# Optimization experiments

Hardware: AMD Instinct MI355X
Metric: run time of the kernel (lower is better)

The kernel has to match this reference:

```python
import jax, jax.numpy as jnp
import numpy as np

BOND_D = 4    # disentangler bond dim (hard-coded 4 in torch init)
BOND_I = 16   # isometry bond dim (bond_dim kwarg)
F = 2         # feature_dim = 2*nCh, nCh=1 -> [x, 1-x] embedding
LEVELS = [128, 64, 32, 16, 8, 4]
NUM_CLASSES = 10
BATCH = 16


def setup_inputs() -> dict:
    key = jax.random.key(0)
    ks = iter(jax.random.split(key, 128))
    inp = {}
    inp["x"] = jax.random.uniform(next(ks), (BATCH, 1, 128, 128), dtype=jnp.float32)

    def mps_params(P, D, O):
        A = 0.2 * jax.random.normal(next(ks), (P, 4, F, D, D), dtype=jnp.float32)
        v = 0.2 * jax.random.normal(next(ks), (P, D), dtype=jnp.float32)
        w = 0.2 * jax.random.normal(next(ks), (P, D, O), dtype=jnp.float32)
        return A, v, w

    for l, H in enumerate(LEVELS, start=1):
        Pd = ((H - 2) // 2) ** 2   # number of disentangler patches
        Pi = (H // 2) ** 2         # number of isometry patches
        inp[f"d{l}A"], inp[f"d{l}v"], inp[f"d{l}w"] = mps_params(Pd, BOND_D, 4)
        inp[f"i{l}A"], inp[f"i{l}v"], inp[f"i{l}w"] = mps_params(Pi, BOND_I, 1)
    inp["fA"], inp["fv"], inp["fw"] = mps_params(1, BOND_I, NUM_CLASSES)
    return inp


def _patches(x):
    # x: [b, H, W] (H, W even) -> [b, (H/2)*(W/2), 4], same site order as
    # torch unfold(2,2,2).unfold(3,2,2).reshape(..., 4)
    b, H, W = x.shape
    return x.reshape(b, H // 2, 2, W // 2, 2).transpose(0, 1, 3, 2, 4).reshape(b, -1, 4)


def _unpatch(y, nh, nw):
    # y: [b, nh*nw, 4] -> [b, 2*nh, 2*nw], inverse spatial placement of 2x2 blocks
    b = y.shape[0]
    return y.reshape(b, nh, nw, 2, 2).transpose(0, 1, 3, 2, 4).reshape(b, 2 * nh, 2 * nw)


def _mps(patches, A, v, w):
    # Batched per-patch ReLU-MPS over 4 sites.
    # patches [b,P,4], A [P,4,F,D,D], v [P,D], w [P,D,O] -> [b,P,O]
    phi = jnp.stack([patches, 1.0 - patches], axis=-1)          # [b,P,4,F]
    M = jnp.einsum('bpsf,psfij->bpsij', phi, A)                 # [b,P,4,D,D]
    vec = jnp.einsum('pi,bpij->bpj', v, M[:, :, 0])             # [b,P,D]
    for s in range(1, 4):
        vec = jnp.einsum('bpi,bpij->bpj', vec, M[:, :, s])
    return jax.nn.relu(jnp.einsum('bpi,pio->bpo', vec, w))


def _level(x, dA, dv, dw, iA, iv, iw):
    # One MERA layer: disentangle shifted interior patches, write back, then
    # isometry-pool the full grid 2x2 -> 1.
    b, H, W = x.shape
    nh = (H - 2) // 2
    y = _mps(_patches(x[:, 1:-1, 1:-1]), dA, dv, dw)            # [b, nh*nh, 4]
    x = x.at[:, 1:-1, 1:-1].set(_unpatch(y, nh, nh))
    y2 = _mps(_patches(x), iA, iv, iw)                          # [b, (H/2)^2, 1]
    return y2.reshape(b, H // 2, W // 2)


def reference(x, d1A, d1v, d1w, i1A, i1v, i1w,
              d2A, d2v, d2w, i2A, i2v, i2w,
              d3A, d3v, d3w, i3A, i3v, i3w,
              d4A, d4v, d4w, i4A, i4v, i4w,
              d5A, d5v, d5w, i5A, i5v, i5w,
              d6A, d6v, d6w, i6A, i6v, i6w,
              fA, fv, fw):
    h = x[:, 0]  # nCh = 1
    levels = [(d1A, d1v, d1w, i1A, i1v, i1w), (d2A, d2v, d2w, i2A, i2v, i2w),
              (d3A, d3v, d3w, i3A, i3v, i3w), (d4A, d4v, d4w, i4A, i4v, i4w),
              (d5A, d5v, d5w, i5A, i5v, i5w), (d6A, d6v, d6w, i6A, i6v, i6w)]
    for p in levels:
        h = _level(h, *p)
    flat = h.reshape(h.shape[0], 1, 4)         # final 2x2 grid -> 4 sites
    return _mps(flat, fA, fv, fw)[:, 0]        # [b, NUM_CLASSES]
```

## Files before the change

### kernel.cpp

```cpp
#include <hip/hip_runtime.h>

#define BATCH 16

template <int CTRL>
__device__ __forceinline__ float qperm(float x) {
  int xi = __float_as_int(x);
  return __int_as_float(__builtin_amdgcn_update_dpp(xi, xi, CTRL, 0xF, 0xF, true));
}

__device__ __forceinline__ float4 f4fma(float s, float4 a, float4 c) {
  c.x = fmaf(s, a.x, c.x);
  c.y = fmaf(s, a.y, c.y);
  c.z = fmaf(s, a.z, c.z);
  c.w = fmaf(s, a.w, c.w);
  return c;
}

__device__ __forceinline__ void mps16_chain(const float* __restrict__ A,
                                            int jq, const float tt[4],
                                            float vec[4]) {
#pragma unroll
  for (int s = 0; s < 4; s++) {
    const float4* A0v = (const float4*)(A + s * 512) + jq;
    const float4* A1v = A0v + 64;
    float4 q0 = {0.f, 0.f, 0.f, 0.f}, q1 = {0.f, 0.f, 0.f, 0.f};
#define ISTEP(i)                                         \
  {                                                      \
    float sv = qperm<(((i) >> 2) * 0x55)>(vec[(i) & 3]); \
    q0 = f4fma(sv, A0v[(i) * 4], q0);                    \
    q1 = f4fma(sv, A1v[(i) * 4], q1);                    \
  }
    ISTEP(0) ISTEP(1) ISTEP(2) ISTEP(3)
    ISTEP(4) ISTEP(5) ISTEP(6) ISTEP(7)
    ISTEP(8) ISTEP(9) ISTEP(10) ISTEP(11)
    ISTEP(12) ISTEP(13) ISTEP(14) ISTEP(15)
#undef ISTEP
    float ph = tt[s], om = 1.0f - ph;
    vec[0] = ph * q0.x + om * q1.x;
    vec[1] = ph * q0.y + om * q1.y;
    vec[2] = ph * q0.z + om * q1.z;
    vec[3] = ph * q0.w + om * q1.w;
  }
}

template <int H, int XS>
__device__ __forceinline__ float fused_di_quad(
    const float* __restrict__ xb, int p, int jq,
    const float* __restrict__ dA, const float* __restrict__ dv,
    const float* __restrict__ dw,
    const float* __restrict__ iA, const float* __restrict__ iv,
    const float* __restrict__ iw) {
  constexpr int NH = (H - 2) / 2;
  constexpr int W2 = H / 2;
  int pi = p / W2, pj = p % W2;
  int r = 2 * pi + (jq >> 1), c = 2 * pj + (jq & 1);
  float tcell;
  bool border = (r == 0) | (r == H - 1) | (c == 0) | (c == H - 1);
  if (border) {
    tcell = xb[(r * H + c) * XS];
  } else {
    int dpi = (r - 1) >> 1, dpj = (c - 1) >> 1;
    int sd = ((r - 1) & 1) * 2 + ((c - 1) & 1);
    int dp = dpi * NH + dpj;
    int R0 = 1 + 2 * dpi, C0 = 1 + 2 * dpj;
    float tins[4];
    tins[0] = xb[(R0 * H + C0) * XS];
    tins[1] = xb[(R0 * H + C0 + 1) * XS];
    tins[2] = xb[((R0 + 1) * H + C0) * XS];
    tins[3] = xb[((R0 + 1) * H + C0 + 1) * XS];
    const float4* Av = (const float4*)(dA + dp * 128);
    float4 dvv = *(const float4*)(dv + dp * 4);
    float v0 = dvv.x, v1 = dvv.y, v2 = dvv.z, v3 = dvv.w;
#pragma unroll
    for (int s = 0; s < 4; s++) {
      const float4* A0 = Av + s * 8;
      float4 q0 = {0.f, 0.f, 0.f, 0.f}, q1 = {0.f, 0.f, 0.f, 0.f};
      q0 = f4fma(v0, A0[0], q0);
      q0 = f4fma(v1, A0[1], q0);
      q0 = f4fma(v2, A0[2], q0);
      q0 = f4fma(v3, A0[3], q0);
      q1 = f4fma(v0, A0[4], q1);
      q1 = f4fma(v1, A0[5], q1);
      q1 = f4fma(v2, A0[6], q1);
      q1 = f4fma(v3, A0[7], q1);
      float ph = tins[s], om = 1.0f - ph;
      v0 = ph * q0.x + om * q1.x;
      v1 = ph * q0.y + om * q1.y;
      v2 = ph * q0.z + om * q1.z;
      v3 = ph * q0.w + om * q1.w;
    }
    const float* wp = dw + dp * 16 + sd;
    float y = v0 * wp[0];
    y = fmaf(v1, wp[4], y);
    y = fmaf(v2, wp[8], y);
    y = fmaf(v3, wp[12], y);
    tcell = fmaxf(y, 0.0f);
  }
  float tt[4];
  tt[0] = qperm<0x00>(tcell);
  tt[1] = qperm<0x55>(tcell);
  tt[2] = qperm<0xAA>(tcell);
  tt[3] = qperm<0xFF>(tcell);
  float4 vv = *(const float4*)(iv + p * 16 + 4 * jq);
  float vec[4] = {vv.x, vv.y, vv.z, vv.w};
  mps16_chain(iA + (size_t)p * 2048, jq, tt, vec);
  float4 wv = *(const float4*)(iw + p * 16 + 4 * jq);
  float partial = vec[0] * wv.x;
  partial = fmaf(vec[1], wv.y, partial);
  partial = fmaf(vec[2], wv.z, partial);
  partial = fmaf(vec[3], wv.w, partial);
  partial += qperm<0xB1>(partial);
  partial += qperm<0x4E>(partial);
  return fmaxf(partial, 0.0f);
}

template <int H, int BP, int XS>
__global__ __launch_bounds__(256) void level_kernel(
    const float* __restrict__ xin, float* __restrict__ hn,
    const float* __restrict__ dA, const float* __restrict__ dv,
    const float* __restrict__ dw, const float* __restrict__ iA,
    const float* __restrict__ iv, const float* __restrict__ iw) {
  int tid = threadIdx.x;
  int jq = tid & 3;
  int b = (tid >> 2) & 15;
  int p = blockIdx.x * BP + (tid >> 6);
  const float* xb = (XS == 1) ? (xin + b * H * H) : (xin + b);
  float o = fused_di_quad<H, XS>(xb, p, jq, dA, dv, dw, iA, iv, iw);
  if (jq == 0) hn[p * 16 + b] = o;
}

struct TailArgs {
  const float* h3;
  const float* in[21];
  float* out;
};

__global__ __launch_bounds__(256) void tail_kernel(TailArgs a) {
  __shared__ float x4[256];
  __shared__ float x5[64];
  __shared__ float x6[16];
  __shared__ float h6[4];
  int b = blockIdx.x;
  int tid = threadIdx.x;
  x4[tid] = a.h3[tid * 16 + b];
  __syncthreads();
  {
    int jq = tid & 3, p = tid >> 2;
    float o = fused_di_quad<16, 1>(x4, p, jq, a.in[0], a.in[1], a.in[2],
                                   a.in[3], a.in[4], a.in[5]);
    if (jq == 0) x5[p] = o;
  }
  __syncthreads();
  if (tid < 64) {
    int jq = tid & 3, p = tid >> 2;
    float o = fused_di_quad<8, 1>(x5, p, jq, a.in[6], a.in[7], a.in[8],
                                  a.in[9], a.in[10], a.in[11]);
    if (jq == 0) x6[p] = o;
  }
  __syncthreads();
  if (tid < 16) {
    int jq = tid & 3, p = tid >> 2;
    float o = fused_di_quad<4, 1>(x6, p, jq, a.in[12], a.in[13], a.in[14],
                                  a.in[15], a.in[16], a.in[17]);
    if (jq == 0) h6[p] = o;
  }
  __syncthreads();
  if (tid < 4) {
    int jq = tid;
    const float* fA = a.in[18];
    const float* fv = a.in[19];
    const float* fw = a.in[20];
    float tt[4] = {h6[0], h6[1], h6[2], h6[3]};
    float4 vv = *(const float4*)(fv + 4 * jq);
    float vec[4] = {vv.x, vv.y, vv.z, vv.w};
    mps16_chain(fA, jq, tt, vec);
    float acc[10];
#pragma unroll
    for (int o = 0; o < 10; o++) acc[o] = 0.f;
#pragma unroll
    for (int k = 0; k < 4; k++)
#pragma unroll
      for (int o = 0; o < 10; o++)
        acc[o] = fmaf(vec[k], fw[(4 * jq + k) * 10 + o], acc[o]);
#pragma unroll
    for (int o = 0; o < 10; o++) {
      acc[o] += qperm<0xB1>(acc[o]);
      acc[o] += qperm<0x4E>(acc[o]);
    }
    if (jq == 0) {
#pragma unroll
      for (int o = 0; o < 10; o++) a.out[b * 10 + o] = fmaxf(acc[o], 0.0f);
    }
  }
}

extern "C" void kernel_launch(void* const* d_in, const int* in_sizes, int n_in,
                              void* d_out, int out_size, void* d_ws, size_t ws_size,
                              hipStream_t stream) {
  const float* x = (const float*)d_in[0];
  float* ws = (float*)d_ws;
  float* h1 = ws;
  float* h2 = h1 + 65536;
  float* h3 = h2 + 16384;

  level_kernel<128, 4, 1><<<1024, 256, 0, stream>>>(
      x, h1, (const float*)d_in[1], (const float*)d_in[2],
      (const float*)d_in[3], (const float*)d_in[4], (const float*)d_in[5],
      (const float*)d_in[6]);
  level_kernel<64, 4, 16><<<256, 256, 0, stream>>>(
      h1, h2, (const float*)d_in[7], (const float*)d_in[8],
      (const float*)d_in[9], (const float*)d_in[10], (const float*)d_in[11],
      (const float*)d_in[12]);
  level_kernel<32, 1, 16><<<256, 64, 0, stream>>>(
      h2, h3, (const float*)d_in[13], (const float*)d_in[14],
      (const float*)d_in[15], (const float*)d_in[16], (const float*)d_in[17],
      (const float*)d_in[18]);

  TailArgs ta;
  ta.h3 = h3;
  for (int i = 0; i < 21; i++) ta.in[i] = (const float*)d_in[19 + i];
  ta.out = (float*)d_out;
  tail_kernel<<<BATCH, 256, 0, stream>>>(ta);
}
```

Baseline: 222.7 us.

## Stage per-block MPS parameters in LDS, transpose input, restructure level/tail kernels

Each level block now cooperatively loads its isometry tensors and the neighbouring disentangler tensors into shared memory with coalesced float4 loads, then runs the chains out of LDS. Previously every thread read scattered global memory. A new transpose kernel puts the input in batch-innermost layout so level 1 can use the same path. Level 4 moves from the single-block-per-batch tail into the grid-wide level kernel, and the tail now handles four batches per block over levels 5-6 and the final MPS. This adds a kernel launch and LDS pressure, and duplicates disentangler loads at block halos.

```diff
diff --git a/kernel.cpp b/kernel.cpp
--- a/kernel.cpp
+++ b/kernel.cpp
@@ -16,9 +16,8 @@
   return c;
 }
 
-__device__ __forceinline__ void mps16_chain(const float* __restrict__ A,
-                                            int jq, const float tt[4],
-                                            float vec[4]) {
+__device__ __forceinline__ void mps16_chain(const float* A, int jq,
+                                            const float tt[4], float vec[4]) {
 #pragma unroll
   for (int s = 0; s < 4; s++) {
     const float4* A0v = (const float4*)(A + s * 512) + jq;
@@ -114,63 +113,212 @@
   return fmaxf(partial, 0.0f);
 }
 
-template <int H, int BP, int XS>
+#define OFF_IA 0
+#define OFF_IV 8192
+#define OFF_IW 8256
+#define OFF_DA 8320
+#define OFF_DV 9640
+#define OFF_DW 9680
+#define LDS_TOT 9840
+
+template <int H>
 __global__ __launch_bounds__(256) void level_kernel(
-    const float* __restrict__ xin, float* __restrict__ hn,
+    const float* __restrict__ xT, float* __restrict__ hn,
     const float* __restrict__ dA, const float* __restrict__ dv,
     const float* __restrict__ dw, const float* __restrict__ iA,
     const float* __restrict__ iv, const float* __restrict__ iw) {
+  constexpr int W2 = H / 2, NH = (H - 2) / 2;
+  __shared__ __align__(16) float lds[LDS_TOT];
+  float4* l4 = (float4*)lds;
+  const int tid = threadIdx.x;
+  const int p0 = blockIdx.x * 4;
+  const int pi = p0 / W2, pj0 = p0 % W2;
+  const int jq = tid & 3, b = (tid >> 2) & 15, w = tid >> 6;
+  const int pj = pj0 + w;
+  const int r = 2 * pi + (jq >> 1), c = 2 * pj + (jq & 1);
+  const bool border = (r == 0) | (r == H - 1) | (c == 0) | (c == H - 1);
+  const int dpi = (r - 1) >> 1, dpj = (c - 1) >> 1;
+
+  float xv0, xv1, xv2, xv3;
+  if (border) {
+    xv0 = xT[(r * H + c) * 16 + b];
+  } else {
+    int R0 = 1 + 2 * dpi, C0 = 1 + 2 * dpj;
+    xv0 = xT[(R0 * H + C0) * 16 + b];
+    xv1 = xT[(R0 * H + C0 + 1) * 16 + b];
+    xv2 = xT[((R0 + 1) * H + C0) * 16 + b];
+    xv3 = xT[((R0 + 1) * H + C0 + 1) * 16 + b];
+  }
+
+  {
+    const float4* iA4 = (const float4*)iA + p0 * 512;
+    float4 ra[8];
+#pragma unroll
+    for (int k = 0; k < 8; k++) ra[k] = iA4[tid + k * 256];
+
+    float4 rd0, rd1;
+    int sl0, gr0, sl1, gr1;
+    const bool md1 = tid < 64;
+    {
+      int g = tid;
+      int rs = g / 160, rem = g % 160, cs = rem / 32;
+      gr0 = rem % 32;
+      int di = min(max(pi - 1 + rs, 0), NH - 1);
+      int dj = min(max(pj0 - 1 + cs, 0), NH - 1);
+      sl0 = rs * 5 + cs;
+      rd0 = *((const float4*)dA + (di * NH + dj) * 32 + gr0);
+    }
+    if (md1) {
+      int g = tid + 256;
+      int rs = g / 160, rem = g % 160, cs = rem / 32;
+      gr1 = rem % 32;
+      int di = min(max(pi - 1 + rs, 0), NH - 1);
+      int dj = min(max(pj0 - 1 + cs, 0), NH - 1);
+      sl1 = rs * 5 + cs;
+      rd1 = *((const float4*)dA + (di * NH + dj) * 32 + gr1);
+    }
+    float4 rv;
+    const bool mv = tid < 10;
+    if (mv) {
+      int rs = tid / 5, cs = tid % 5;
+      int di = min(max(pi - 1 + rs, 0), NH - 1);
+      int dj = min(max(pj0 - 1 + cs, 0), NH - 1);
+      rv = *((const float4*)dv + (di * NH + dj));
+    }
+    float4 rw;
+    const bool mw = tid < 40;
+    if (mw) {
+      int rs = tid / 20, rem = tid % 20, cs = rem / 4, gr = rem % 4;
+      int di = min(max(pi - 1 + rs, 0), NH - 1);
+      int dj = min(max(pj0 - 1 + cs, 0), NH - 1);
+      rw = *((const float4*)dw + (di * NH + dj) * 4 + gr);
+    }
+    float4 rvv, rww;
+    const bool mi = tid < 16;
+    if (mi) {
+      rvv = *((const float4*)iv + p0 * 4 + tid);
+      rww = *((const float4*)iw + p0 * 4 + tid);
+    }
+#pragma unroll
+    for (int k = 0; k < 8; k++) l4[OFF_IA / 4 + tid + k * 256] = ra[k];
+    l4[OFF_DA / 4 + sl0 * 33 + gr0] = rd0;
+    if (md1) l4[OFF_DA / 4 + sl1 * 33 + gr1] = rd1;
+    if (mv) l4[OFF_DV / 4 + tid] = rv;
+    if (mw) l4[OFF_DW / 4 + tid] = rw;
+    if (mi) l4[OFF_IV / 4 + tid] = rvv;
+    if (mi) l4[OFF_IW / 4 + tid] = rww;
+  }
+  __syncthreads();
+
+  float tcell;
+  if (border) {
+    tcell = xv0;
+  } else {
+    int sd = ((r - 1) & 1) * 2 + ((c - 1) & 1);
+    int slot = (dpi - pi + 1) * 5 + (dpj - pj0 + 1);
+    const float4* Av = (const float4*)(lds + OFF_DA + slot * 132);
+    float4 dvv = *(const float4*)(lds + OFF_DV + slot * 4);
+    float v0 = dvv.x, v1 = dvv.y, v2 = dvv.z, v3 = dvv.w;
+    float tins[4] = {xv0, xv1, xv2, xv3};
+#pragma unroll
+    for (int s = 0; s < 4; s++) {
+      const float4* A0 = Av + s * 8;
+      float4 q0 = {0.f, 0.f, 0.f, 0.f}, q1 = {0.f, 0.f, 0.f, 0.f};
+      q0 = f4fma(v0, A0[0], q0);
+      q0 = f4fma(v1, A0[1], q0);
+      q0 = f4fma(v2, A0[2], q0);
+      q0 = f4fma(v3, A0[3], q0);
+      q1 = f4fma(v0, A0[4], q1);
+      q1 = f4fma(v1, A0[5], q1);
+      q1 = f4fma(v2, A0[6], q1);
+      q1 = f4fma(v3, A0[7], q1);
+      float ph = tins[s], om = 1.0f - ph;
+      v0 = ph * q0.x + om * q1.x;
+      v1 = ph * q0.y + om * q1.y;
+      v2 = ph * q0.z + om * q1.z;
+      v3 = ph * q0.w + om * q1.w;
+    }
+    const float* wp = lds + OFF_DW + slot * 16 + sd;
+    float y = v0 * wp[0];
+    y = fmaf(v1, wp[4], y);
+    y = fmaf(v2, wp[8], y);
+    y = fmaf(v3, wp[12], y);
+    tcell = fmaxf(y, 0.0f);
+  }
+  float tt[4];
+  tt[0] = qperm<0x00>(tcell);
+  tt[1] = qperm<0x55>(tcell);
+  tt[2] = qperm<0xAA>(tcell);
+  tt[3] = qperm<0xFF>(tcell);
+  float4 vv = *(const float4*)(lds + OFF_IV + w * 16 + 4 * jq);
+  float vec[4] = {vv.x, vv.y, vv.z, vv.w};
+  mps16_chain(lds + OFF_IA + w * 2048, jq, tt, vec);
+  float4 wv = *(const float4*)(lds + OFF_IW + w * 16 + 4 * jq);
+  float partial = vec[0] * wv.x;
+  partial = fmaf(vec[1], wv.y, partial);
+  partial = fmaf(vec[2], wv.z, partial);
+  partial = fmaf(vec[3], wv.w, partial);
+  partial += qperm<0xB1>(partial);
+  partial += qperm<0x4E>(partial);
+  if (jq == 0) hn[(p0 + w) * 16 + b] = fmaxf(partial, 0.0f);
+}
+
+__global__ __launch_bounds__(256) void transpose_kernel(
+    const float* __restrict__ x, float* __restrict__ xT) {
+  __shared__ float t[64][17];
   int tid = threadIdx.x;
-  int jq = tid & 3;
-  int b = (tid >> 2) & 15;
-  int p = blockIdx.x * BP + (tid >> 6);
-  const float* xb = (XS == 1) ? (xin + b * H * H) : (xin + b);
-  float o = fused_di_quad<H, XS>(xb, p, jq, dA, dv, dw, iA, iv, iw);
-  if (jq == 0) hn[p * 16 + b] = o;
+  int c0 = blockIdx.x * 64;
+  {
+    int bb = tid >> 4, c4 = tid & 15;
+    float4 v = *((const float4*)(x + bb * 16384 + c0) + c4);
+    t[c4 * 4 + 0][bb] = v.x;
+    t[c4 * 4 + 1][bb] = v.y;
+    t[c4 * 4 + 2][bb] = v.z;
+    t[c4 * 4 + 3][bb] = v.w;
+  }
+  __syncthreads();
+  {
+    int cl = tid >> 2, bq = tid & 3;
+    float4 v;
+    v.x = t[cl][bq * 4 + 0];
+    v.y = t[cl][bq * 4 + 1];
+    v.z = t[cl][bq * 4 + 2];
+    v.w = t[cl][bq * 4 + 3];
+    *((float4*)(xT + (c0 + cl) * 16) + bq) = v;
+  }
 }
 
 struct TailArgs {
-  const float* h3;
-  const float* in[21];
+  const float* h4;
+  const float* in[15];
   float* out;
 };
 
-__global__ __launch_bounds__(256) void tail_kernel(TailArgs a) {
-  __shared__ float x4[256];
-  __shared__ float x5[64];
-  __shared__ float x6[16];
-  __shared__ float h6[4];
-  int b = blockIdx.x;
+__global__ __launch_bounds__(256) void tail2_kernel(TailArgs a) {
+  __shared__ float h5l[4][16];
+  __shared__ float h6l[4][4];
   int tid = threadIdx.x;
-  x4[tid] = a.h3[tid * 16 + b];
-  __syncthreads();
   {
-    int jq = tid & 3, p = tid >> 2;
-    float o = fused_di_quad<16, 1>(x4, p, jq, a.in[0], a.in[1], a.in[2],
+    int jq = tid & 3, p = (tid >> 2) & 15, bl = tid >> 6;
+    int b = blockIdx.x * 4 + bl;
+    float o = fused_di_quad<8, 16>(a.h4 + b, p, jq, a.in[0], a.in[1], a.in[2],
                                    a.in[3], a.in[4], a.in[5]);
-    if (jq == 0) x5[p] = o;
+    if (jq == 0) h5l[bl][p] = o;
   }
   __syncthreads();
   if (tid < 64) {
-    int jq = tid & 3, p = tid >> 2;
-    float o = fused_di_quad<8, 1>(x5, p, jq, a.in[6], a.in[7], a.in[8],
-                                  a.in[9], a.in[10], a.in[11]);
-    if (jq == 0) x6[p] = o;
+    int jq = tid & 3, p = (tid >> 2) & 3, bl = tid >> 4;
+    float o = fused_di_quad<4, 1>(&h5l[bl][0], p, jq, a.in[6], a.in[7],
+                                  a.in[8], a.in[9], a.in[10], a.in[11]);
+    if (jq == 0) h6l[bl][p] = o;
   }
   __syncthreads();
   if (tid < 16) {
-    int jq = tid & 3, p = tid >> 2;
-    float o = fused_di_quad<4, 1>(x6, p, jq, a.in[12], a.in[13], a.in[14],
-                                  a.in[15], a.in[16], a.in[17]);
-    if (jq == 0) h6[p] = o;
-  }
-  __syncthreads();
-  if (tid < 4) {
-    int jq = tid;
-    const float* fA = a.in[18];
-    const float* fv = a.in[19];
-    const float* fw = a.in[20];
-    float tt[4] = {h6[0], h6[1], h6[2], h6[3]};
+    int jq = tid & 3, bl = tid >> 2;
+    const float* fA = a.in[12];
+    const float* fv = a.in[13];
+    const float* fw = a.in[14];
+    float tt[4] = {h6l[bl][0], h6l[bl][1], h6l[bl][2], h6l[bl][3]};
     float4 vv = *(const float4*)(fv + 4 * jq);
     float vec[4] = {vv.x, vv.y, vv.z, vv.w};
     mps16_chain(fA, jq, tt, vec);
@@ -188,6 +336,7 @@
       acc[o] += qperm<0x4E>(acc[o]);
     }
     if (jq == 0) {
+      int b = blockIdx.x * 4 + bl;
 #pragma unroll
       for (int o = 0; o < 10; o++) a.out[b * 10 + o] = fmaxf(acc[o], 0.0f);
     }
@@ -199,26 +348,33 @@
                               hipStream_t stream) {
   const float* x = (const float*)d_in[0];
   float* ws = (float*)d_ws;
-  float* h1 = ws;
+  float* xT = ws;
+  float* h1 = xT + 262144;
   float* h2 = h1 + 65536;
   float* h3 = h2 + 16384;
-
-  level_kernel<128, 4, 1><<<1024, 256, 0, stream>>>(
-      x, h1, (const float*)d_in[1], (const float*)d_in[2],
+  float* h4 = h3 + 4096;
+
+  transpose_kernel<<<256, 256, 0, stream>>>(x, xT);
+  level_kernel<128><<<1024, 256, 0, stream>>>(
+      xT, h1, (const float*)d_in[1], (const float*)d_in[2],
       (const float*)d_in[3], (const float*)d_in[4], (const float*)d_in[5],
       (const float*)d_in[6]);
-  level_kernel<64, 4, 16><<<256, 256, 0, stream>>>(
+  level_kernel<64><<<256, 256, 0, stream>>>(
       h1, h2, (const float*)d_in[7], (const float*)d_in[8],
       (const float*)d_in[9], (const float*)d_in[10], (const float*)d_in[11],
       (const float*)d_in[12]);
-  level_kernel<32, 1, 16><<<256, 64, 0, stream>>>(
+  level_kernel<32><<<64, 256, 0, stream>>>(
       h2, h3, (const float*)d_in[13], (const float*)d_in[14],
       (const float*)d_in[15], (const float*)d_in[16], (const float*)d_in[17],
       (const float*)d_in[18]);
+  level_kernel<16><<<16, 256, 0, stream>>>(
+      h3, h4, (const float*)d_in[19], (const float*)d_in[20],
+      (const float*)d_in[21], (const float*)d_in[22], (const float*)d_in[23],
+      (const float*)d_in[24]);
 
   TailArgs ta;
-  ta.h3 = h3;
-  for (int i = 0; i < 21; i++) ta.in[i] = (const float*)d_in[19 + i];
+  ta.h4 = h4;
+  for (int i = 0; i < 15; i++) ta.in[i] = (const float*)d_in[25 + i];
   ta.out = (float*)d_out;
-  tail_kernel<<<BATCH, 256, 0, stream>>>(ta);
-}
+  tail2_kernel<<<4, 256, 0, stream>>>(ta);
+}
```

Result: faster. 195.5 us (-12.2%).
